# Optimization experiments

Measured on AMD Instinct MI355X. Metric: run time of the kernel, lower is better.

The kernel has to match this reference:

```python
import jax, jax.numpy as jnp
import numpy as np

B, N_REG, D_IN = 32, 116, 256
N_NODES = B * N_REG            # 3712
E_PER_G = N_REG * 10           # avg degree 10
E = B * E_PER_G                # 37120
HEADS = 8
HID = [256, 128, 64]
D_OUT = 256
LN_EPS = 1e-5


def _layer_norm(x, scale, bias):
    mu = x.mean(-1, keepdims=True)
    var = ((x - mu) ** 2).mean(-1, keepdims=True)
    return (x - mu) * jax.lax.rsqrt(var + LN_EPS) * scale + bias


def _gat_layer(x, W, b, a_src, a_dst, src, dst, concat):
    """PyG-style GATConv (shared lin, self-loops, leaky_relu 0.2) + ELU + LayerNorm."""
    N = x.shape[0]
    H, C = a_src.shape
    h = (x @ W).reshape(N, H, C)                      # (N, H, C)
    sl = jnp.arange(N, dtype=src.dtype)               # self-loops (PyG default)
    s = jnp.concatenate([src, sl])
    d = jnp.concatenate([dst, sl])
    al = (h * a_src).sum(-1)                          # (N, H)
    ar = (h * a_dst).sum(-1)                          # (N, H)
    e = jax.nn.leaky_relu(al[s] + ar[d], 0.2)         # (E', H)
    m = jax.ops.segment_max(e, d, num_segments=N)
    ex = jnp.exp(e - m[d])
    den = jax.ops.segment_sum(ex, d, num_segments=N)
    alpha = ex / den[d]                               # segment softmax over incoming edges
    out = jax.ops.segment_sum(h[s] * alpha[..., None], d, num_segments=N)  # (N, H, C)
    out = out.reshape(N, H * C) if concat else out.mean(1)
    return out + b


def setup_inputs() -> dict:
    key = jax.random.key(0)
    ks = list(jax.random.split(key, 32))
    node_features = jax.random.normal(ks[0], (N_NODES, D_IN), dtype=jnp.float32)
    # edges: random within each graph (disconnected batched graph)
    off = (jnp.arange(B, dtype=jnp.int32) * N_REG)[:, None]
    src = (jax.random.randint(ks[1], (B, E_PER_G), 0, N_REG, dtype=jnp.int32) + off).reshape(-1)
    dst = (jax.random.randint(ks[2], (B, E_PER_G), 0, N_REG, dtype=jnp.int32) + off).reshape(-1)
    batch = jnp.repeat(jnp.arange(B, dtype=jnp.int32), N_REG)

    def lin(k, fin, fout):
        s = 1.0 / np.sqrt(fin)
        return jax.random.uniform(k, (fin, fout), jnp.float32, -s, s)

    dims_in = [D_IN, HID[0] * HEADS, HID[1] * HEADS]
    p = {}
    ki = 3
    for i, (fin, c) in enumerate(zip(dims_in, HID)):
        concat = i < len(HID) - 1
        wdim = c * HEADS
        p[f"w{i}"] = lin(ks[ki], fin, wdim); ki += 1
        p[f"b{i}"] = jnp.zeros((wdim if concat else c,), jnp.float32)
        p[f"as{i}"] = jax.random.normal(ks[ki], (HEADS, c), jnp.float32) * 0.1; ki += 1
        p[f"ad{i}"] = jax.random.normal(ks[ki], (HEADS, c), jnp.float32) * 0.1; ki += 1
        ldim = wdim if concat else c
        p[f"ls{i}"] = jnp.ones((ldim,), jnp.float32)
        p[f"lb{i}"] = jnp.zeros((ldim,), jnp.float32)
    p["wp"] = lin(ks[ki], HID[-1], D_OUT); ki += 1
    p["bp"] = jnp.zeros((D_OUT,), jnp.float32)
    p["lsp"] = jnp.ones((D_OUT,), jnp.float32)
    p["lbp"] = jnp.zeros((D_OUT,), jnp.float32)
    p["wq"] = lin(ks[ki], D_OUT, 1); ki += 1
    p["bq"] = jnp.zeros((1,), jnp.float32)
    return dict(node_features=node_features, src=src, dst=dst, batch=batch, **p)


def reference(node_features, src, dst, batch,
              w0, b0, as0, ad0, ls0, lb0,
              w1, b1, as1, ad1, ls1, lb1,
              w2, b2, as2, ad2, ls2, lb2,
              wp, bp, lsp, lbp, wq, bq):
    x = node_features
    x = _layer_norm(jax.nn.elu(_gat_layer(x, w0, b0, as0, ad0, src, dst, True)), ls0, lb0)
    x = _layer_norm(jax.nn.elu(_gat_layer(x, w1, b1, as1, ad1, src, dst, True)), ls1, lb1)
    x = _layer_norm(jax.nn.elu(_gat_layer(x, w2, b2, as2, ad2, src, dst, False)), ls2, lb2)
    node_out = jax.nn.gelu(_layer_norm(x @ wp + bp, lsp, lbp), approximate=False)  # (N, 256)
    pool_w = jax.nn.softmax(node_out @ wq + bq, axis=0)                            # (N, 1) global softmax
    num = jax.ops.segment_sum(node_out * pool_w, batch, num_segments=B)            # (B, 256)
    den = jnp.maximum(jax.ops.segment_sum(pool_w, batch, num_segments=B), 1e-8)    # (B, 1)
    graph_features = num / den
    return graph_features, node_out
```

## Files before the change

kernel.cpp:

```cpp
#include <hip/hip_runtime.h>
#include <hip/hip_bf16.h>
#include <math.h>

typedef __hip_bfloat16 bf16;
typedef short short8 __attribute__((ext_vector_type(8)));
typedef float f32x4 __attribute__((ext_vector_type(4)));

__device__ __forceinline__ float b2f(const bf16 v) { return __bfloat162float(v); }
__device__ __forceinline__ bf16 f2b(const float v) { return __float2bfloat16(v); }

__device__ __forceinline__ float bits2f(short s) {
  unsigned u = ((unsigned)(unsigned short)s) << 16;
  float f;
  __builtin_memcpy(&f, &u, 4);
  return f;
}
__device__ __forceinline__ short f2bits(float f) {
  bf16 b = f2b(f);
  short s;
  __builtin_memcpy(&s, &b, 2);
  return s;
}

__device__ __forceinline__ float ldsel(const void* p, size_t i, int f32) {
  return f32 ? ((const float*)p)[i] : b2f(((const bf16*)p)[i]);
}
__device__ __forceinline__ void stsel(void* p, size_t i, float v, int f32) {
  if (f32) ((float*)p)[i] = v; else ((bf16*)p)[i] = f2b(v);
}

#define NN 3712
#define NE 37120
#define NG 32
#define NREG 116
#define MAXDEG 48

__global__ __launch_bounds__(256) void k_detect(const void* nf, const void* w0, int* flags) {
  __shared__ int bad[2];
  if (threadIdx.x < 2) bad[threadIdx.x] = 0;
  __syncthreads();
  const bf16* a = (const bf16*)nf;
  const bf16* b = (const bf16*)w0;
  int l0 = 0, l1 = 0;
  for (int i = threadIdx.x; i < 4096; i += 256) {
    float x = b2f(a[i]); if (!(fabsf(x) < 1e4f)) l0++;
    float y = b2f(b[i]); if (!(fabsf(y) < 1e4f)) l1++;
  }
  if (l0) atomicAdd(&bad[0], l0);
  if (l1) atomicAdd(&bad[1], l1);
  __syncthreads();
  if (threadIdx.x == 0) { flags[0] = bad[0] > 0; flags[1] = bad[1] > 0; }
}

__global__ __launch_bounds__(256) void k_zero(int* __restrict__ p, int n) {
  int i = blockIdx.x * 256 + threadIdx.x;
  if (i < n) p[i] = 0;
}

__global__ __launch_bounds__(256) void k_scatter(const int* __restrict__ src, const int* __restrict__ dst,
                                                 int* __restrict__ cnt, int* __restrict__ bucket, int E) {
  int e = blockIdx.x * 256 + threadIdx.x;
  if (e < E) {
    int d = dst[e], s = src[e];
    if ((unsigned)d < NN && (unsigned)s < NN) {
      int p = atomicAdd(&cnt[d], 1);
      if (p < MAXDEG) bucket[d * MAXDEG + p] = s;
    }
  }
}

__global__ __launch_bounds__(256) void k_tobf16(const void* __restrict__ in, bf16* __restrict__ out,
                                                int n, const int* __restrict__ flags, int fidx) {
  int f = flags[fidx];
  int i = blockIdx.x * 256 + threadIdx.x;
  if (i < n) out[i] = f2b(ldsel(in, i, f));
}

__global__ __launch_bounds__(256) void k_transpose(const void* __restrict__ W, bf16* __restrict__ Wt,
                                                   int K, int N, const int* __restrict__ flags) {
  int f = flags[1];
  __shared__ float tile[32][33];
  int tx = threadIdx.x & 31, ty = threadIdx.x >> 5;
  int k0 = blockIdx.x * 32, n0 = blockIdx.y * 32;
#pragma unroll
  for (int i = 0; i < 4; ++i)
    tile[ty + i * 8][tx] = ldsel(W, (size_t)(k0 + ty + i * 8) * N + n0 + tx, f);
  __syncthreads();
#pragma unroll
  for (int i = 0; i < 4; ++i)
    Wt[(size_t)(n0 + ty + i * 8) * K + k0 + tx] = f2b(tile[tx][ty + i * 8]);
}

__global__ __launch_bounds__(256) void k_gemm_mfma(const bf16* __restrict__ A, const bf16* __restrict__ Bt,
                                                   bf16* __restrict__ C, int M, int N, int K) {
  __shared__ short As[64 * 72];
  __shared__ short Bs[64 * 72];
  int tid = threadIdx.x;
  int wave = tid >> 6, lane = tid & 63;
  int wr = wave >> 1, wc = wave & 1;
  int quad = lane >> 4, ml = lane & 15;

  int nbx = N >> 6;
  int total = gridDim.x;
  int id = blockIdx.x;
  int tile = ((total & 7) == 0) ? ((id & 7) * (total >> 3) + (id >> 3)) : id;
  int n0 = (tile % nbx) << 6;
  int m0 = (tile / nbx) << 6;

  f32x4 acc[2][2];
#pragma unroll
  for (int rt = 0; rt < 2; ++rt)
#pragma unroll
    for (int ct = 0; ct < 2; ++ct)
#pragma unroll
      for (int r = 0; r < 4; ++r) acc[rt][ct][r] = 0.f;

  for (int k0 = 0; k0 < K; k0 += 64) {
    __syncthreads();
#pragma unroll
    for (int i = 0; i < 2; ++i) {
      int c = tid + (i << 8);
      int row = c >> 3, kg = (c & 7) << 3;
      *(uint4*)&As[row * 72 + kg] = *(const uint4*)&A[(size_t)(m0 + row) * K + k0 + kg];
      *(uint4*)&Bs[row * 72 + kg] = *(const uint4*)&Bt[(size_t)(n0 + row) * K + k0 + kg];
    }
    __syncthreads();
    short8 af[2][2], bfr[2][2];
#pragma unroll
    for (int rt = 0; rt < 2; ++rt)
#pragma unroll
      for (int kk = 0; kk < 2; ++kk)
        af[rt][kk] = *(const short8*)&As[(wr * 32 + rt * 16 + ml) * 72 + kk * 32 + quad * 8];
#pragma unroll
    for (int ct = 0; ct < 2; ++ct)
#pragma unroll
      for (int kk = 0; kk < 2; ++kk)
        bfr[ct][kk] = *(const short8*)&Bs[(wc * 32 + ct * 16 + ml) * 72 + kk * 32 + quad * 8];
#pragma unroll
    for (int rt = 0; rt < 2; ++rt)
#pragma unroll
      for (int ct = 0; ct < 2; ++ct)
#pragma unroll
        for (int kk = 0; kk < 2; ++kk)
          acc[rt][ct] = __builtin_amdgcn_mfma_f32_16x16x32_bf16(af[rt][kk], bfr[ct][kk], acc[rt][ct], 0, 0, 0);
  }
#pragma unroll
  for (int rt = 0; rt < 2; ++rt)
#pragma unroll
    for (int ct = 0; ct < 2; ++ct)
#pragma unroll
      for (int r = 0; r < 4; ++r) {
        int grow = m0 + wr * 32 + rt * 16 + quad * 4 + r;
        int gcol = n0 + wc * 32 + ct * 16 + ml;
        C[(size_t)grow * N + gcol] = f2b(acc[rt][ct][r]);
      }
}

__global__ __launch_bounds__(256) void k_attn(const bf16* __restrict__ H, const void* __restrict__ a_s,
                                              const void* __restrict__ a_d, float* __restrict__ al,
                                              float* __restrict__ ar, int C, const int* __restrict__ flags) {
  int wF = flags[1];
  int n = blockIdx.x;
  int t = threadIdx.x;
  int D = 8 * C;
  int i0 = t * 8;
  if (i0 >= D) return;
  union { short8 v; short s[8]; } u;
  u.v = *(const short8*)&H[(size_t)n * D + i0];
  float ps = 0.f, pd = 0.f;
#pragma unroll
  for (int j = 0; j < 8; ++j) {
    float h = bits2f(u.s[j]);
    ps = fmaf(h, ldsel(a_s, i0 + j, wF), ps);
    pd = fmaf(h, ldsel(a_d, i0 + j, wF), pd);
  }
  int G = C >> 3;
  for (int off = G >> 1; off; off >>= 1) {
    ps += __shfl_xor(ps, off);
    pd += __shfl_xor(pd, off);
  }
  if ((t & (G - 1)) == 0) {
    int hd = i0 / C;
    al[n * 8 + hd] = ps;
    ar[n * 8 + hd] = pd;
  }
}

__global__ __launch_bounds__(256) void k_agg(const bf16* __restrict__ H, const float* __restrict__ al,
                                             const float* __restrict__ ar, const int* __restrict__ cnt,
                                             const int* __restrict__ bucket, const void* __restrict__ bias,
                                             const void* __restrict__ ls, const void* __restrict__ lb,
                                             bf16* __restrict__ Xout, int C, int concat,
                                             const int* __restrict__ flags) {
  int wF = flags[1];
  int bid = blockIdx.x;
  int x = bid & 7, jj = bid >> 3;
  int d = (x + ((jj / NREG) << 3)) * NREG + (jj % NREG);
  int t = threadIdx.x;
  int lane = t & 63, wave = t >> 6;
  int D = 8 * C;
  __shared__ int sid[MAXDEG + 1];
  __shared__ float w[8][MAXDEG + 2];
  __shared__ float vals[512];
  __shared__ float r1[4], r2[4];
  __shared__ float sMu, sRs;

  int deg = cnt[d]; deg = deg > MAXDEG ? MAXDEG : deg;
  if (t < deg) sid[t] = bucket[d * MAXDEG + t];
  if (t == deg) sid[deg] = d;
  __syncthreads();
  int total = deg + 1;

  if (t < 64) {
    int hd = t >> 3, le = t & 7;
    float ard = ar[d * 8 + hd];
    float m = -1e30f;
    for (int e = le; e < total; e += 8) {
      float lg = al[sid[e] * 8 + hd] + ard;
      lg = lg > 0.f ? lg : 0.2f * lg;
      w[hd][e] = lg;
      m = fmaxf(m, lg);
    }
#pragma unroll
    for (int off = 4; off; off >>= 1) m = fmaxf(m, __shfl_xor(m, off));
    float den = 0.f;
    for (int e = le; e < total; e += 8) { float xv = expf(w[hd][e] - m); w[hd][e] = xv; den += xv; }
#pragma unroll
    for (int off = 4; off; off >>= 1) den += __shfl_xor(den, off);
    float inv = 1.f / den;
    for (int e = le; e < total; e += 8) w[hd][e] *= inv;
  }
  __syncthreads();

  int i0 = t * 8;
  float acc[8] = {0.f, 0.f, 0.f, 0.f, 0.f, 0.f, 0.f, 0.f};
  if (i0 < D) {
    int hd = i0 / C;
    const bf16* __restrict__ Hp = H + i0;
    for (int e = 0; e < total; ++e) {
      union { short8 v; short s[8]; } u;
      u.v = *(const short8*)&Hp[(size_t)sid[e] * D];
      float we = w[hd][e];
#pragma unroll
      for (int j = 0; j < 8; ++j) acc[j] = fmaf(we, bits2f(u.s[j]), acc[j]);
    }
  }

  if (concat) {
    float v[8];
    float s1 = 0.f, s2 = 0.f;
    if (i0 < D) {
#pragma unroll
      for (int j = 0; j < 8; ++j) {
        float vv = acc[j] + ldsel(bias, i0 + j, wF);
        vv = vv > 0.f ? vv : expf(vv) - 1.f;
        v[j] = vv; s1 += vv; s2 += vv * vv;
      }
    }
#pragma unroll
    for (int off = 32; off; off >>= 1) { s1 += __shfl_down(s1, off); s2 += __shfl_down(s2, off); }
    if (lane == 0) { r1[wave] = s1; r2[wave] = s2; }
    __syncthreads();
    if (t == 0) {
      float S1 = r1[0] + r1[1] + r1[2] + r1[3];
      float S2 = r2[0] + r2[1] + r2[2] + r2[3];
      float mu = S1 / D;
      sMu = mu; sRs = rsqrtf(S2 / D - mu * mu + 1e-5f);
    }
    __syncthreads();
    if (i0 < D) {
      union { short8 v; short s[8]; } ou;
#pragma unroll
      for (int j = 0; j < 8; ++j)
        ou.s[j] = f2bits((v[j] - sMu) * sRs * ldsel(ls, i0 + j, wF) + ldsel(lb, i0 + j, wF));
      *(short8*)&Xout[(size_t)d * D + i0] = ou.v;
    }
  } else {
    if (i0 < D) {
#pragma unroll
      for (int j = 0; j < 8; ++j) vals[i0 + j] = acc[j];
    }
    __syncthreads();
    if (t < 64) {
      float v = 0.f;
#pragma unroll
      for (int h = 0; h < 8; ++h) v += vals[h * 64 + t];
      v = v * 0.125f + ldsel(bias, t, wF);
      v = v > 0.f ? v : expf(v) - 1.f;
      float s1 = v, s2 = v * v;
#pragma unroll
      for (int off = 32; off; off >>= 1) { s1 += __shfl_xor(s1, off); s2 += __shfl_xor(s2, off); }
      float mu = s1 * (1.f / 64.f);
      float var = s2 * (1.f / 64.f) - mu * mu;
      float rs = rsqrtf(var + 1e-5f);
      Xout[(size_t)d * 64 + t] = f2b((v - mu) * rs * ldsel(ls, t, wF) + ldsel(lb, t, wF));
    }
  }
}

__global__ __launch_bounds__(256) void k_proj(const bf16* __restrict__ X3, const void* __restrict__ wp,
                                              const void* __restrict__ bp, const void* __restrict__ lsp,
                                              const void* __restrict__ lbp, const void* __restrict__ wq,
                                              const void* __restrict__ bq,
                                              float* __restrict__ q, void* __restrict__ dout,
                                              const int* __restrict__ flags) {
  int wF = flags[1], xF = flags[0];
  int n = blockIdx.x, t = threadIdx.x;
  int lane = t & 63, wave = t >> 6;
  __shared__ float xs[64];
  __shared__ float r1[4], r2[4];
  __shared__ float sMu, sRs;
  if (t < 64) xs[t] = b2f(X3[n * 64 + t]);
  __syncthreads();
  float y = ldsel(bp, t, wF);
#pragma unroll 8
  for (int k = 0; k < 64; ++k) y = fmaf(xs[k], ldsel(wp, k * 256 + t, wF), y);
  float s1 = y, s2 = y * y;
#pragma unroll
  for (int off = 32; off; off >>= 1) { s1 += __shfl_down(s1, off); s2 += __shfl_down(s2, off); }
  if (lane == 0) { r1[wave] = s1; r2[wave] = s2; }
  __syncthreads();
  if (t == 0) {
    float S1 = r1[0] + r1[1] + r1[2] + r1[3];
    float S2 = r2[0] + r2[1] + r2[2] + r2[3];
    float mu = S1 / 256.f;
    sMu = mu; sRs = rsqrtf(S2 / 256.f - mu * mu + 1e-5f);
  }
  __syncthreads();
  float v = (y - sMu) * sRs * ldsel(lsp, t, wF) + ldsel(lbp, t, wF);
  float g = 0.5f * v * (1.f + erff(v * 0.70710678118654752f));
  stsel(dout, (size_t)NG * 256 + (size_t)n * 256 + t, g, xF);
  float qv = g * ldsel(wq, t, wF);
#pragma unroll
  for (int off = 32; off; off >>= 1) qv += __shfl_down(qv, off);
  if (lane == 0) r1[wave] = qv;
  __syncthreads();
  if (t == 0) q[n] = r1[0] + r1[1] + r1[2] + r1[3] + ldsel(bq, 0, wF);
}

__global__ __launch_bounds__(256) void k_pool(void* __restrict__ dout, const float* __restrict__ q,
                                              const int* __restrict__ flags) {
  int xF = flags[0];
  int b = blockIdx.x, t = threadIdx.x;
  __shared__ float es[NREG];
  __shared__ float sDen;
  if (t < NREG) es[t] = q[b * NREG + t];
  __syncthreads();
  if (t == 0) {
    float m = -1e30f;
    for (int i = 0; i < NREG; ++i) m = fmaxf(m, es[i]);
    float den = 0.f;
    for (int i = 0; i < NREG; ++i) { float e = expf(es[i] - m); es[i] = e; den += e; }
    sDen = den;
  }
  __syncthreads();
  float acc = 0.f;
  for (int i = 0; i < NREG; ++i)
    acc = fmaf(es[i], ldsel(dout, (size_t)NG * 256 + (size_t)(b * NREG + i) * 256 + t, xF), acc);
  stsel(dout, (size_t)b * 256 + t, acc / sDen, xF);
}

extern "C" void kernel_launch(void* const* d_in, const int* in_sizes, int n_in,
                              void* d_out, int out_size, void* d_ws, size_t ws_size,
                              hipStream_t stream) {
  const void* nf  = d_in[0];
  const int* src  = (const int*)d_in[1];
  const int* dst  = (const int*)d_in[2];
  const void *w0 = d_in[4],  *b0 = d_in[5],  *as0 = d_in[6], *ad0 = d_in[7],  *ls0 = d_in[8],  *lb0 = d_in[9];
  const void *w1 = d_in[10], *b1 = d_in[11], *as1 = d_in[12], *ad1 = d_in[13], *ls1 = d_in[14], *lb1 = d_in[15];
  const void *w2 = d_in[16], *b2 = d_in[17], *as2 = d_in[18], *ad2 = d_in[19], *ls2 = d_in[20], *lb2 = d_in[21];
  const void *wp = d_in[22], *bp = d_in[23], *lsp = d_in[24], *lbp = d_in[25], *wq = d_in[26], *bq = d_in[27];

  int* flags  = (int*)d_ws;
  float* al   = (float*)(flags + 4);
  float* ar   = al + NN * 8;
  int* cnt    = (int*)(ar + NN * 8);
  int* bucket = cnt + NN;
  float* q    = (float*)(bucket + NN * MAXDEG);
  bf16* X     = (bf16*)(q + NN);
  bf16* Hb    = X + (size_t)NN * 2048;

  bf16* X0  = X;
  bf16* wt0 = X + (1 << 20);
  bf16* wt1 = Hb + (size_t)NN * 1024;
  bf16* wt2 = Hb + (size_t)NN * 512;

  k_detect<<<1, 256, 0, stream>>>(nf, w0, flags);
  k_zero<<<(NN + 255) / 256, 256, 0, stream>>>(cnt, NN);
  k_scatter<<<(NE + 255) / 256, 256, 0, stream>>>(src, dst, cnt, bucket, NE);
  k_tobf16<<<(NN * 256 + 255) / 256, 256, 0, stream>>>(nf, X0, NN * 256, flags, 0);

  k_transpose<<<dim3(256 / 32, 2048 / 32), 256, 0, stream>>>(w0, wt0, 256, 2048, flags);
  k_gemm_mfma<<<(2048 / 64) * (NN / 64), 256, 0, stream>>>(X0, wt0, Hb, NN, 2048, 256);
  k_attn<<<NN, 256, 0, stream>>>(Hb, as0, ad0, al, ar, 256, flags);
  k_agg<<<NN, 256, 0, stream>>>(Hb, al, ar, cnt, bucket, b0, ls0, lb0, X, 256, 1, flags);

  k_transpose<<<dim3(2048 / 32, 1024 / 32), 256, 0, stream>>>(w1, wt1, 2048, 1024, flags);
  k_gemm_mfma<<<(1024 / 64) * (NN / 64), 256, 0, stream>>>(X, wt1, Hb, NN, 1024, 2048);
  k_attn<<<NN, 256, 0, stream>>>(Hb, as1, ad1, al, ar, 128, flags);
  k_agg<<<NN, 256, 0, stream>>>(Hb, al, ar, cnt, bucket, b1, ls1, lb1, X, 128, 1, flags);

  k_transpose<<<dim3(1024 / 32, 512 / 32), 256, 0, stream>>>(w2, wt2, 1024, 512, flags);
  k_gemm_mfma<<<(512 / 64) * (NN / 64), 256, 0, stream>>>(X, wt2, Hb, NN, 512, 1024);
  k_attn<<<NN, 256, 0, stream>>>(Hb, as2, ad2, al, ar, 64, flags);
  k_agg<<<NN, 256, 0, stream>>>(Hb, al, ar, cnt, bucket, b2, ls2, lb2, X, 64, 0, flags);

  k_proj<<<NN, 256, 0, stream>>>(X, wp, bp, lsp, lbp, wq, bq, q, d_out, flags);
  k_pool<<<NG, 256, 0, stream>>>(d_out, q, flags);
}
```

Baseline: 387.1 us.

## Right-size aggregation blocks, distribute softmax across threads, batch neighbor gathers

Launches k_attn and k_agg with block sizes matching the feature width (128 or 64 threads for the later layers) so no idle threads are scheduled. The edge softmax is now computed by every thread group per head instead of only the first 64 threads, which removes one barrier. The neighbor list is padded to a multiple of 8 with zero-weight self entries so eight row gathers can be issued before accumulating, giving more memory-level parallelism. The padding adds a few redundant loads, and the k_attn launch with fewer threads relies on that kernel already handling any block size.

```diff
diff --git a/kernel.cpp b/kernel.cpp
--- a/kernel.cpp
+++ b/kernel.cpp
@@ -186,115 +186,111 @@
   }
 }
 
-__global__ __launch_bounds__(256) void k_agg(const bf16* __restrict__ H, const float* __restrict__ al,
-                                             const float* __restrict__ ar, const int* __restrict__ cnt,
-                                             const int* __restrict__ bucket, const void* __restrict__ bias,
-                                             const void* __restrict__ ls, const void* __restrict__ lb,
-                                             bf16* __restrict__ Xout, int C, int concat,
-                                             const int* __restrict__ flags) {
+__global__ void k_agg(const bf16* __restrict__ H, const float* __restrict__ al,
+                      const float* __restrict__ ar, const int* __restrict__ cnt,
+                      const int* __restrict__ bucket, const void* __restrict__ bias,
+                      const void* __restrict__ ls, const void* __restrict__ lb,
+                      bf16* __restrict__ Xout, int C, int concat,
+                      const int* __restrict__ flags) {
   int wF = flags[1];
   int bid = blockIdx.x;
   int x = bid & 7, jj = bid >> 3;
   int d = (x + ((jj / NREG) << 3)) * NREG + (jj % NREG);
   int t = threadIdx.x;
+  int nt = blockDim.x;
   int lane = t & 63, wave = t >> 6;
   int D = 8 * C;
-  __shared__ int sid[MAXDEG + 1];
-  __shared__ float w[8][MAXDEG + 2];
+  __shared__ int sid[MAXDEG + 8];
+  __shared__ float w[8][MAXDEG + 8];
   __shared__ float vals[512];
   __shared__ float r1[4], r2[4];
   __shared__ float sMu, sRs;
 
   int deg = cnt[d]; deg = deg > MAXDEG ? MAXDEG : deg;
+  int total = deg + 1;
+  int padded = (total + 7) & ~7;
   if (t < deg) sid[t] = bucket[d * MAXDEG + t];
-  if (t == deg) sid[deg] = d;
-  __syncthreads();
-  int total = deg + 1;
-
-  if (t < 64) {
-    int hd = t >> 3, le = t & 7;
-    float ard = ar[d * 8 + hd];
-    float m = -1e30f;
-    for (int e = le; e < total; e += 8) {
-      float lg = al[sid[e] * 8 + hd] + ard;
-      lg = lg > 0.f ? lg : 0.2f * lg;
-      w[hd][e] = lg;
-      m = fmaxf(m, lg);
-    }
-#pragma unroll
-    for (int off = 4; off; off >>= 1) m = fmaxf(m, __shfl_xor(m, off));
-    float den = 0.f;
-    for (int e = le; e < total; e += 8) { float xv = expf(w[hd][e] - m); w[hd][e] = xv; den += xv; }
-#pragma unroll
-    for (int off = 4; off; off >>= 1) den += __shfl_xor(den, off);
-    float inv = 1.f / den;
-    for (int e = le; e < total; e += 8) w[hd][e] *= inv;
-  }
+  else if (t < padded) sid[t] = d;
   __syncthreads();
 
   int i0 = t * 8;
+  int hd = i0 / C;
+  int G = C >> 3;
+  int gl = t & (G - 1);
+  float ard = ar[d * 8 + hd];
+  float m = -1e30f;
+  for (int e = gl; e < total; e += G) {
+    float lg = al[sid[e] * 8 + hd] + ard;
+    lg = lg > 0.f ? lg : 0.2f * lg;
+    w[hd][e] = lg;
+    m = fmaxf(m, lg);
+  }
+  for (int off = G >> 1; off; off >>= 1) m = fmaxf(m, __shfl_xor(m, off));
+  float den = 0.f;
+  for (int e = gl; e < total; e += G) { float xv = expf(w[hd][e] - m); w[hd][e] = xv; den += xv; }
+  for (int off = G >> 1; off; off >>= 1) den += __shfl_xor(den, off);
+  float inv = 1.f / den;
+  for (int e = gl; e < total; e += G) w[hd][e] *= inv;
+  if (gl < padded - total) w[hd][total + gl] = 0.f;
+
   float acc[8] = {0.f, 0.f, 0.f, 0.f, 0.f, 0.f, 0.f, 0.f};
-  if (i0 < D) {
-    int hd = i0 / C;
-    const bf16* __restrict__ Hp = H + i0;
-    for (int e = 0; e < total; ++e) {
-      union { short8 v; short s[8]; } u;
-      u.v = *(const short8*)&Hp[(size_t)sid[e] * D];
-      float we = w[hd][e];
-#pragma unroll
-      for (int j = 0; j < 8; ++j) acc[j] = fmaf(we, bits2f(u.s[j]), acc[j]);
+  const bf16* __restrict__ Hp = H + i0;
+  for (int eb = 0; eb < padded; eb += 8) {
+    short8 u[8];
+#pragma unroll
+    for (int j = 0; j < 8; ++j)
+      u[j] = *(const short8*)&Hp[(size_t)sid[eb + j] * D];
+#pragma unroll
+    for (int j = 0; j < 8; ++j) {
+      float we = w[hd][eb + j];
+      union { short8 v; short s[8]; } uu; uu.v = u[j];
+#pragma unroll
+      for (int k = 0; k < 8; ++k) acc[k] = fmaf(we, bits2f(uu.s[k]), acc[k]);
     }
   }
 
   if (concat) {
     float v[8];
     float s1 = 0.f, s2 = 0.f;
-    if (i0 < D) {
-#pragma unroll
-      for (int j = 0; j < 8; ++j) {
-        float vv = acc[j] + ldsel(bias, i0 + j, wF);
-        vv = vv > 0.f ? vv : expf(vv) - 1.f;
-        v[j] = vv; s1 += vv; s2 += vv * vv;
-      }
+#pragma unroll
+    for (int j = 0; j < 8; ++j) {
+      float vv = acc[j] + ldsel(bias, i0 + j, wF);
+      vv = vv > 0.f ? vv : expf(vv) - 1.f;
+      v[j] = vv; s1 += vv; s2 += vv * vv;
     }
 #pragma unroll
     for (int off = 32; off; off >>= 1) { s1 += __shfl_down(s1, off); s2 += __shfl_down(s2, off); }
     if (lane == 0) { r1[wave] = s1; r2[wave] = s2; }
     __syncthreads();
     if (t == 0) {
-      float S1 = r1[0] + r1[1] + r1[2] + r1[3];
-      float S2 = r2[0] + r2[1] + r2[2] + r2[3];
+      float S1 = 0.f, S2 = 0.f;
+      int nw = nt >> 6;
+      for (int i = 0; i < nw; ++i) { S1 += r1[i]; S2 += r2[i]; }
       float mu = S1 / D;
       sMu = mu; sRs = rsqrtf(S2 / D - mu * mu + 1e-5f);
     }
     __syncthreads();
-    if (i0 < D) {
-      union { short8 v; short s[8]; } ou;
-#pragma unroll
-      for (int j = 0; j < 8; ++j)
-        ou.s[j] = f2bits((v[j] - sMu) * sRs * ldsel(ls, i0 + j, wF) + ldsel(lb, i0 + j, wF));
-      *(short8*)&Xout[(size_t)d * D + i0] = ou.v;
-    }
+    union { short8 v; short s[8]; } ou;
+#pragma unroll
+    for (int j = 0; j < 8; ++j)
+      ou.s[j] = f2bits((v[j] - sMu) * sRs * ldsel(ls, i0 + j, wF) + ldsel(lb, i0 + j, wF));
+    *(short8*)&Xout[(size_t)d * D + i0] = ou.v;
   } else {
-    if (i0 < D) {
-#pragma unroll
-      for (int j = 0; j < 8; ++j) vals[i0 + j] = acc[j];
-    }
+#pragma unroll
+    for (int j = 0; j < 8; ++j) vals[i0 + j] = acc[j];
     __syncthreads();
-    if (t < 64) {
-      float v = 0.f;
-#pragma unroll
-      for (int h = 0; h < 8; ++h) v += vals[h * 64 + t];
-      v = v * 0.125f + ldsel(bias, t, wF);
-      v = v > 0.f ? v : expf(v) - 1.f;
-      float s1 = v, s2 = v * v;
-#pragma unroll
-      for (int off = 32; off; off >>= 1) { s1 += __shfl_xor(s1, off); s2 += __shfl_xor(s2, off); }
-      float mu = s1 * (1.f / 64.f);
-      float var = s2 * (1.f / 64.f) - mu * mu;
-      float rs = rsqrtf(var + 1e-5f);
-      Xout[(size_t)d * 64 + t] = f2b((v - mu) * rs * ldsel(ls, t, wF) + ldsel(lb, t, wF));
-    }
+    float v = 0.f;
+#pragma unroll
+    for (int h = 0; h < 8; ++h) v += vals[h * 64 + t];
+    v = v * 0.125f + ldsel(bias, t, wF);
+    v = v > 0.f ? v : expf(v) - 1.f;
+    float s1 = v, s2 = v * v;
+#pragma unroll
+    for (int off = 32; off; off >>= 1) { s1 += __shfl_xor(s1, off); s2 += __shfl_xor(s2, off); }
+    float mu = s1 * (1.f / 64.f);
+    float var = s2 * (1.f / 64.f) - mu * mu;
+    float rs = rsqrtf(var + 1e-5f);
+    Xout[(size_t)d * 64 + t] = f2b((v - mu) * rs * ldsel(ls, t, wF) + ldsel(lb, t, wF));
   }
 }
 
@@ -397,13 +393,13 @@
 
   k_transpose<<<dim3(2048 / 32, 1024 / 32), 256, 0, stream>>>(w1, wt1, 2048, 1024, flags);
   k_gemm_mfma<<<(1024 / 64) * (NN / 64), 256, 0, stream>>>(X, wt1, Hb, NN, 1024, 2048);
-  k_attn<<<NN, 256, 0, stream>>>(Hb, as1, ad1, al, ar, 128, flags);
-  k_agg<<<NN, 256, 0, stream>>>(Hb, al, ar, cnt, bucket, b1, ls1, lb1, X, 128, 1, flags);
+  k_attn<<<NN, 128, 0, stream>>>(Hb, as1, ad1, al, ar, 128, flags);
+  k_agg<<<NN, 128, 0, stream>>>(Hb, al, ar, cnt, bucket, b1, ls1, lb1, X, 128, 1, flags);
 
   k_transpose<<<dim3(1024 / 32, 512 / 32), 256, 0, stream>>>(w2, wt2, 1024, 512, flags);
   k_gemm_mfma<<<(512 / 64) * (NN / 64), 256, 0, stream>>>(X, wt2, Hb, NN, 512, 1024);
-  k_attn<<<NN, 256, 0, stream>>>(Hb, as2, ad2, al, ar, 64, flags);
-  k_agg<<<NN, 256, 0, stream>>>(Hb, al, ar, cnt, bucket, b2, ls2, lb2, X, 64, 0, flags);
+  k_attn<<<NN, 64, 0, stream>>>(Hb, as2, ad2, al, ar, 64, flags);
+  k_agg<<<NN, 64, 0, stream>>>(Hb, al, ar, cnt, bucket, b2, ls2, lb2, X, 64, 0, flags);
 
   k_proj<<<NN, 256, 0, stream>>>(X, wp, bp, lsp, lbp, wq, bq, q, d_out, flags);
   k_pool<<<NG, 256, 0, stream>>>(d_out, q, flags);
```

After: 386.2 us. Within noise of the previous version (-0.3%).
